# Kernel optimization log

Hardware: AMD Instinct MI355X
Metric: run time of the kernel (lower is better)

The kernel has to match this reference:

```python
import jax, jax.numpy as jnp
import numpy as np

B = 262144
N_FEAT = 256
N_D = 64
N_A = 64
N_OUT = N_D + N_A  # 128
N_STEPS = 3
N_STEP_DEP = 2
VBS = 1024
GAMMA = 1.3
EPS_BN = 1e-5
SQRT_HALF = float(np.sqrt(0.5))


def _xavier(key, shape):
    fan_in, fan_out = shape[-2], shape[-1]
    return (jax.random.normal(key, shape) * np.sqrt(2.0 / (fan_in + fan_out))).astype(jnp.float32)


def setup_inputs() -> dict:
    key = jax.random.key(0)
    ks = jax.random.split(key, 8)
    return {
        "x": jax.random.normal(ks[0], (B, N_FEAT), dtype=jnp.float32),
        "bn0_g": jnp.ones((N_FEAT,), jnp.float32),
        "bn0_b": jnp.zeros((N_FEAT,), jnp.float32),
        "W_sh0": _xavier(ks[1], (N_FEAT, 2 * N_OUT)),
        "g_sh0": jnp.ones((2 * N_OUT,), jnp.float32),
        "b_sh0": jnp.zeros((2 * N_OUT,), jnp.float32),
        "W_sh1": _xavier(ks[2], (N_OUT, 2 * N_OUT)),
        "g_sh1": jnp.ones((2 * N_OUT,), jnp.float32),
        "b_sh1": jnp.zeros((2 * N_OUT,), jnp.float32),
        "W_step": _xavier(ks[3], (N_STEPS, N_STEP_DEP, N_OUT, 2 * N_OUT)),
        "g_step": jnp.ones((N_STEPS, N_STEP_DEP, 2 * N_OUT), jnp.float32),
        "b_step": jnp.zeros((N_STEPS, N_STEP_DEP, 2 * N_OUT), jnp.float32),
        "W_att": _xavier(ks[4], (N_STEPS, N_A, N_FEAT)),
        "g_att": jnp.ones((N_STEPS, N_FEAT), jnp.float32),
        "b_att": jnp.zeros((N_STEPS, N_FEAT), jnp.float32),
    }


def batch_norm(x, g, b):
    # training-mode BN over the full batch (biased variance, as torch)
    mu = x.mean(0)
    var = ((x - mu) ** 2).mean(0)
    return (x - mu) * jax.lax.rsqrt(var + EPS_BN) * g + b


def ghost_bn(x, g, b):
    # split batch into virtual sub-batches of VBS and BN each chunk
    n, f = x.shape
    xr = x.reshape(n // VBS, VBS, f)
    mu = xr.mean(1, keepdims=True)
    var = ((xr - mu) ** 2).mean(1, keepdims=True)
    xn = (xr - mu) * jax.lax.rsqrt(var + EPS_BN)
    return xn.reshape(n, f) * g + b


def sparsemax(z):
    zs = jnp.flip(jnp.sort(z, axis=-1), axis=-1)      # descending
    cs = jnp.cumsum(zs, axis=-1)
    n = z.shape[-1]
    k = jnp.arange(1, n + 1, dtype=z.dtype)
    support = (k * zs > cs - 1.0).astype(z.dtype)
    kz = support.sum(-1, keepdims=True)
    idx = jnp.clip(kz - 1.0, 0.0).astype(jnp.int32)
    tau = (jnp.take_along_axis(cs, idx, axis=-1) - 1.0) / kz
    return jnp.maximum(z - tau, 0.0)


def glu(x, W, g, b):
    h = ghost_bn(x @ W, g, b)
    h1, h2 = jnp.split(h, 2, axis=-1)
    return h1 * jax.nn.sigmoid(h2)


def feat_transformer(x, W_sh0, g_sh0, b_sh0, W_sh1, g_sh1, b_sh1, Wst, gst, bst):
    h = glu(x, W_sh0, g_sh0, b_sh0)
    h = (h + glu(h, W_sh1, g_sh1, b_sh1)) * SQRT_HALF
    for j in range(N_STEP_DEP):
        h = (h + glu(h, Wst[j], gst[j], bst[j])) * SQRT_HALF
    return h


def reference(x, bn0_g, bn0_b, W_sh0, g_sh0, b_sh0, W_sh1, g_sh1, b_sh1,
              W_step, g_step, b_step, W_att, g_att, b_att):
    x_bn = batch_norm(x, bn0_g, bn0_b)
    prior = jnp.ones((B, N_FEAT), x.dtype)
    h_a = jnp.zeros((B, N_A), x.dtype)
    d_out = jnp.zeros((B, N_D), x.dtype)
    sl = jnp.asarray(0.0, x.dtype)
    masks = []
    for s in range(N_STEPS):
        a = ghost_bn(h_a @ W_att[s], g_att[s], b_att[s])
        M = sparsemax(prior * a)
        masks.append(M)
        prior = prior * (GAMMA - M)
        h = feat_transformer(M * x_bn, W_sh0, g_sh0, b_sh0, W_sh1, g_sh1, b_sh1,
                             W_step[s], g_step[s], b_step[s])
        d_out = d_out + jax.nn.relu(h[:, :N_D])
        h_a = h[:, N_D:]
        sl = sl + (-M * jnp.log(M + 1e-15)).mean()
    sl = sl / N_STEPS
    return d_out, sl, jnp.stack(masks)
```

## Files before the change

kernel.cpp:

```cpp
#include <hip/hip_runtime.h>
#include <math.h>

#define B_ROWS 262144
#define GAMMA_C 1.3f
#define EPS_C 1e-5f
#define SQH_C 0.70710678118654752440f
#define SL_SCALE (1.0f/201326592.0f)

typedef _Float16 f16;
typedef f16 f16x8 __attribute__((ext_vector_type(8)));
typedef f16 f16x4 __attribute__((ext_vector_type(4)));
typedef float f32x4 __attribute__((ext_vector_type(4)));

__device__ __forceinline__ int SWZ(int row, int kb, int RB, int MSK) {
  return row * RB + (kb ^ ((row & MSK) << 4));
}

__global__ void bn0_accum(const float* __restrict__ x, float* __restrict__ sums) {
  const int col = threadIdx.x;
  const size_t r0 = (size_t)blockIdx.x * 128;
  float s1 = 0.f, s2 = 0.f;
  for (int i = 0; i < 128; ++i) {
    float v = x[(r0 + i) * 256 + col];
    s1 += v; s2 += v * v;
  }
  atomicAdd(&sums[col * 2], s1);
  atomicAdd(&sums[col * 2 + 1], s2);
}

__global__ void bn0_final(const float* __restrict__ sums, const float* __restrict__ g,
                          const float* __restrict__ b, float* __restrict__ bnA,
                          float* __restrict__ bnB) {
  int c = threadIdx.x;
  float mu = sums[c * 2] * (1.f / B_ROWS);
  float var = sums[c * 2 + 1] * (1.f / B_ROWS) - mu * mu;
  float a = rsqrtf(var + EPS_C) * g[c];
  bnA[c] = a;
  bnB[c] = b[c] - mu * a;
}

__global__ void wprep(const float* __restrict__ src, f16* __restrict__ dst, int K) {
  int idx = blockIdx.x * 256 + threadIdx.x;
  int n = idx / K, k = idx - n * K;
  dst[idx] = (f16)src[(size_t)k * 256 + n];
}

__global__ void m0_kernel(const float* __restrict__ ba, float* __restrict__ m0v,
                          float* __restrict__ prior1v, float* __restrict__ slpart) {
  const int l = threadIdx.x;
  const int c0 = l << 2;
  float z[4];
#pragma unroll
  for (int j = 0; j < 4; ++j) z[j] = ba[c0 + j];
  float m = fmaxf(fmaxf(z[0], z[1]), fmaxf(z[2], z[3]));
#pragma unroll
  for (int d = 1; d < 64; d <<= 1) m = fmaxf(m, __shfl_xor(m, d));
  float lo = m - 1.f, hi = m;
  for (int it = 0; it < 24; ++it) {
    float tau = 0.5f * (lo + hi);
    float s = fmaxf(z[0] - tau, 0.f) + fmaxf(z[1] - tau, 0.f) +
              fmaxf(z[2] - tau, 0.f) + fmaxf(z[3] - tau, 0.f);
#pragma unroll
    for (int d = 1; d < 64; d <<= 1) s += __shfl_xor(s, d);
    if (s > 1.f) lo = tau; else hi = tau;
  }
  const float tau = 0.5f * (lo + hi);
  float ent = 0.f;
#pragma unroll
  for (int j = 0; j < 4; ++j) {
    float M = fmaxf(z[j] - tau, 0.f);
    m0v[c0 + j] = M;
    prior1v[c0 + j] = GAMMA_C - M;
    ent -= M * __logf(M + 1e-15f);
  }
#pragma unroll
  for (int d = 1; d < 64; d <<= 1) ent += __shfl_xor(ent, d);
  if (l == 0) slpart[512] = ent * (262144.f * SL_SCALE);
}

__global__ void mx0_kernel(const float* __restrict__ x, const float* __restrict__ m0v,
                           const float* __restrict__ bnA, const float* __restrict__ bnB,
                           float* __restrict__ mk, f16* __restrict__ Mx) {
  __shared__ float sm[256], sa[256], sb[256];
  const int tid = threadIdx.x;
  sm[tid] = m0v[tid]; sa[tid] = bnA[tid]; sb[tid] = bnB[tid];
  __syncthreads();
  const size_t r = (size_t)blockIdx.x * 8 + (tid >> 5);
  const int c0 = (tid & 31) << 3;
  const float* xp = x + r * 256 + c0;
  f32x4 x0 = *(const f32x4*)xp;
  f32x4 x1 = *(const f32x4*)(xp + 4);
  float* mp = mk + r * 256 + c0;
  f16x8 mxv;
#pragma unroll
  for (int j = 0; j < 4; ++j) {
    mp[j] = sm[c0 + j];
    mp[4 + j] = sm[c0 + 4 + j];
    mxv[j] = (f16)(sm[c0 + j] * (x0[j] * sa[c0 + j] + sb[c0 + j]));
    mxv[4 + j] = (f16)(sm[c0 + 4 + j] * (x1[j] * sa[c0 + 4 + j] + sb[c0 + 4 + j]));
  }
  *(f16x8*)(Mx + r * 256 + c0) = mxv;
}

template <int KD, int RESID, int DOUT>
__launch_bounds__(1024, 4)
__global__ void fglu(const f16* __restrict__ Ag, const f16* __restrict__ Wt,
                     const float* __restrict__ gv, const float* __restrict__ bv,
                     f16* __restrict__ ho, float* __restrict__ dout, int s) {
  constexpr int KS = KD / 32;
  constexpr int RB = KD * 2;
  constexpr int MSK = (RB / 16 - 1) < 31 ? (RB / 16 - 1) : 31;
  constexpr int SPT = (KD == 256) ? 2 : 1;
  constexpr int TPR = KD / 8;
  __shared__ __align__(16) f16 sA[64 * KD];
  __shared__ float sS1[512], sS2[512], sAf[256], sBf[256];
  char* sAc = (char*)sA;
  const int tid = threadIdx.x;
  const int w = tid >> 6, l = tid & 63, lg = l >> 4, lc = l & 15;
  const int mw = w >> 3, nw = w & 7;
  const int c1 = nw * 16 + lc, c2 = c1 + 128;
  const int r0 = blockIdx.x << 10;

  f16x8 bf0[KS], bf1[KS];
#pragma unroll
  for (int ks = 0; ks < KS; ++ks) {
    bf0[ks] = *(const f16x8*)(Wt + (size_t)c1 * KD + ks * 32 + lg * 8);
    bf1[ks] = *(const f16x8*)(Wt + (size_t)c2 * KD + ks * 32 + lg * 8);
  }

  f16x8 pv[SPT];
  auto LDA = [&](int ch) {
#pragma unroll
    for (int p = 0; p < SPT; ++p) {
      int flat = p * 1024 + tid;
      int row = flat / TPR, kc = flat % TPR;
      pv[p] = *(const f16x8*)(Ag + (size_t)(r0 + ch * 64 + row) * KD + kc * 8);
    }
  };
  auto STA = [&]() {
#pragma unroll
    for (int p = 0; p < SPT; ++p) {
      int flat = p * 1024 + tid;
      int row = flat / TPR, kc = flat % TPR;
      *(f16x8*)(sAc + SWZ(row, kc * 16, RB, MSK)) = pv[p];
    }
  };

  float st1a = 0.f, st2a = 0.f, st1b = 0.f, st2b = 0.f;
  LDA(0);
  for (int ch = 0; ch < 16; ++ch) {
    __syncthreads();
    STA();
    __syncthreads();
    if (ch < 15) LDA(ch + 1);
#pragma unroll
    for (int mt = 0; mt < 2; ++mt) {
      f32x4 a0 = {0.f,0.f,0.f,0.f}, a1 = {0.f,0.f,0.f,0.f};
      const int ar = mw * 32 + mt * 16 + lc;
#pragma unroll
      for (int ks = 0; ks < KS; ++ks) {
        f16x8 af = *(const f16x8*)(sAc + SWZ(ar, ks * 64 + lg * 16, RB, MSK));
        a0 = __builtin_amdgcn_mfma_f32_16x16x32_f16(af, bf0[ks], a0, 0, 0, 0);
        a1 = __builtin_amdgcn_mfma_f32_16x16x32_f16(af, bf1[ks], a1, 0, 0, 0);
      }
#pragma unroll
      for (int j = 0; j < 4; ++j) {
        st1a += a0[j]; st2a += a0[j] * a0[j];
        st1b += a1[j]; st2b += a1[j] * a1[j];
      }
    }
  }
  st1a += __shfl_xor(st1a, 16); st1a += __shfl_xor(st1a, 32);
  st2a += __shfl_xor(st2a, 16); st2a += __shfl_xor(st2a, 32);
  st1b += __shfl_xor(st1b, 16); st1b += __shfl_xor(st1b, 32);
  st2b += __shfl_xor(st2b, 16); st2b += __shfl_xor(st2b, 32);
  if (l < 16) {
    sS1[mw * 256 + c1] = st1a; sS2[mw * 256 + c1] = st2a;
    sS1[mw * 256 + c2] = st1b; sS2[mw * 256 + c2] = st2b;
  }
  __syncthreads();
  if (tid < 256) {
    float s1 = sS1[tid] + sS1[256 + tid];
    float s2 = sS2[tid] + sS2[256 + tid];
    float mu = s1 * (1.f / 1024.f);
    float var = s2 * (1.f / 1024.f) - mu * mu;
    float a = rsqrtf(var + EPS_C) * gv[tid];
    sAf[tid] = a; sBf[tid] = bv[tid] - mu * a;
  }
  __syncthreads();
  const float bA1 = sAf[c1], bO1 = sBf[c1], bA2 = sAf[c2], bO2 = sBf[c2];

  LDA(0);
  for (int ch = 0; ch < 16; ++ch) {
    __syncthreads();
    STA();
    __syncthreads();
    if (ch < 15) LDA(ch + 1);
#pragma unroll
    for (int mt = 0; mt < 2; ++mt) {
      f32x4 a0 = {0.f,0.f,0.f,0.f}, a1 = {0.f,0.f,0.f,0.f};
      const int ar = mw * 32 + mt * 16 + lc;
#pragma unroll
      for (int ks = 0; ks < KS; ++ks) {
        f16x8 af = *(const f16x8*)(sAc + SWZ(ar, ks * 64 + lg * 16, RB, MSK));
        a0 = __builtin_amdgcn_mfma_f32_16x16x32_f16(af, bf0[ks], a0, 0, 0, 0);
        a1 = __builtin_amdgcn_mfma_f32_16x16x32_f16(af, bf1[ks], a1, 0, 0, 0);
      }
#pragma unroll
      for (int j = 0; j < 4; ++j) {
        float g1 = a0[j] * bA1 + bO1;
        float g2 = a1[j] * bA2 + bO2;
        float hv = g1 / (1.f + __expf(-g2));
        const int rl = mw * 32 + mt * 16 + lg * 4 + j;
        if (RESID) {
          f16 hp = *(const f16*)(sAc + SWZ(rl, c1 * 2, RB, MSK));
          hv = (hv + (float)hp) * SQH_C;
        }
        if (DOUT && nw < 4) {
          float rv = fmaxf(hv, 0.f);
          float* dp = dout + (size_t)(r0 + ch * 64 + rl) * 64 + c1;
          if (s == 0) *dp = rv; else *dp += rv;
        }
        ho[(size_t)(r0 + ch * 64 + rl) * 128 + c1] = (f16)hv;
      }
    }
  }
}

template <int SMODE>
__launch_bounds__(512)
__global__ void attmask(const f16* __restrict__ h1, const f16* __restrict__ Wt,
                        const float* __restrict__ ga, const float* __restrict__ ba,
                        const float* __restrict__ bnA, const float* __restrict__ bnB,
                        const float* __restrict__ prior1v, const f16* __restrict__ prin,
                        f16* __restrict__ prout, const float* __restrict__ x,
                        float* __restrict__ mk, f16* __restrict__ Mx,
                        float* __restrict__ slpart) {
  __shared__ f16 sW[256 * 64];
  __shared__ f16 sA[128 * 64];
  __shared__ float sS1[256], sS2[256], sAf[256], sBf[256], sbA[256], sbB[256], spv[256];
  __shared__ float sEnt[8];
  char* sWc = (char*)sW;
  char* sAc = (char*)sA;
  const int tid = threadIdx.x;
  const int vb = blockIdx.x;
  const int r0 = vb << 10;
  const int w = tid >> 6, l = tid & 63, lc = l & 15, lg = l >> 4;
  if (tid < 256) {
    sS1[tid] = 0.f; sS2[tid] = 0.f;
    sbA[tid] = bnA[tid]; sbB[tid] = bnB[tid];
    if (SMODE == 1) spv[tid] = prior1v[tid];
  }
#pragma unroll
  for (int it = 0; it < 4; ++it) {
    int flat = it * 512 + tid;
    int rw = flat >> 3, kc = flat & 7;
    *(f16x8*)(sWc + SWZ(rw, kc * 16, 128, 7)) = *(const f16x8*)(Wt + rw * 64 + kc * 8);
  }
  const int arow = tid >> 3, akc = tid & 7;
  const f16* aB = h1 + (size_t)(r0 + arow) * 128 + 64 + akc * 8;
  float ent = 0.f;

  for (int pass = 0; pass < 2; ++pass) {
    float st1[16], st2[16];
#pragma unroll
    for (int t = 0; t < 16; ++t) { st1[t] = 0.f; st2[t] = 0.f; }
    f16x8 pv0 = *(const f16x8*)(aB);
    f16x8 pv1 = *(const f16x8*)(aB + (size_t)64 * 128);
    for (int ch = 0; ch < 8; ++ch) {
      __syncthreads();
      *(f16x8*)(sAc + SWZ(arow, akc * 16, 128, 7)) = pv0;
      *(f16x8*)(sAc + SWZ(arow + 64, akc * 16, 128, 7)) = pv1;
      __syncthreads();
      if (ch + 1 < 8) {
        pv0 = *(const f16x8*)(aB + (size_t)(ch + 1) * 128 * 128);
        pv1 = *(const f16x8*)(aB + (size_t)((ch + 1) * 128 + 64) * 128);
      }
      f16x8 af0 = *(const f16x8*)(sAc + SWZ(w * 16 + lc, lg * 16, 128, 7));
      f16x8 af1 = *(const f16x8*)(sAc + SWZ(w * 16 + lc, 64 + lg * 16, 128, 7));
      const int rb = r0 + ch * 128 + w * 16;
      f32x4 z[16];
#pragma unroll
      for (int t = 0; t < 16; ++t) {
        f16x8 b0 = *(const f16x8*)(sWc + SWZ(t * 16 + lc, lg * 16, 128, 7));
        f16x8 b1 = *(const f16x8*)(sWc + SWZ(t * 16 + lc, 64 + lg * 16, 128, 7));
        f32x4 acc = {0.f, 0.f, 0.f, 0.f};
        acc = __builtin_amdgcn_mfma_f32_16x16x32_f16(af0, b0, acc, 0, 0, 0);
        acc = __builtin_amdgcn_mfma_f32_16x16x32_f16(af1, b1, acc, 0, 0, 0);
        if (pass == 0) {
          float s1 = 0.f, s2 = 0.f;
#pragma unroll
          for (int j = 0; j < 4; ++j) { float v = acc[j]; s1 += v; s2 += v * v; }
          st1[t] += s1; st2[t] += s2;
        } else {
          const int c = t * 16 + lc;
          const float a = sAf[c], bb = sBf[c];
#pragma unroll
          for (int j = 0; j < 4; ++j) {
            float pr;
            if (SMODE == 1) pr = spv[c];
            else pr = (float)prin[(size_t)(rb + lg * 4 + j) * 256 + c];
            z[t][j] = (acc[j] * a + bb) * pr;
          }
        }
      }
      if (pass == 1) {
        f32x4 mj, lo, hi;
#pragma unroll
        for (int j = 0; j < 4; ++j) {
          float m = z[0][j];
#pragma unroll
          for (int t = 1; t < 16; ++t) m = fmaxf(m, z[t][j]);
          mj[j] = m;
        }
#pragma unroll
        for (int d = 1; d < 16; d <<= 1)
#pragma unroll
          for (int j = 0; j < 4; ++j) mj[j] = fmaxf(mj[j], __shfl_xor(mj[j], d));
#pragma unroll
        for (int j = 0; j < 4; ++j) { lo[j] = mj[j] - 1.f; hi[j] = mj[j]; }
        for (int itb = 0; itb < 20; ++itb) {
          f32x4 tau, sv;
#pragma unroll
          for (int j = 0; j < 4; ++j) { tau[j] = 0.5f * (lo[j] + hi[j]); sv[j] = 0.f; }
#pragma unroll
          for (int t = 0; t < 16; ++t)
#pragma unroll
            for (int j = 0; j < 4; ++j) sv[j] += fmaxf(z[t][j] - tau[j], 0.f);
#pragma unroll
          for (int d = 1; d < 16; d <<= 1)
#pragma unroll
            for (int j = 0; j < 4; ++j) sv[j] += __shfl_xor(sv[j], d);
#pragma unroll
          for (int j = 0; j < 4; ++j) { if (sv[j] > 1.f) lo[j] = tau[j]; else hi[j] = tau[j]; }
        }
        f32x4 tau;
#pragma unroll
        for (int j = 0; j < 4; ++j) tau[j] = 0.5f * (lo[j] + hi[j]);
#pragma unroll
        for (int t = 0; t < 16; ++t) {
          const int c = t * 16 + lc;
#pragma unroll
          for (int j = 0; j < 4; ++j) {
            const size_t r = (size_t)(rb + lg * 4 + j);
            float Mv = fmaxf(z[t][j] - tau[j], 0.f);
            mk[r * 256 + c] = Mv;
            ent -= Mv * __logf(Mv + 1e-15f);
            float xb = x[r * 256 + c] * sbA[c] + sbB[c];
            Mx[r * 256 + c] = (f16)(Mv * xb);
            if (SMODE == 1) prout[r * 256 + c] = (f16)(spv[c] * (GAMMA_C - Mv));
          }
        }
      }
    }
    if (pass == 0) {
#pragma unroll
      for (int t = 0; t < 16; ++t) {
        float v1 = st1[t], v2 = st2[t];
        v1 += __shfl_xor(v1, 16); v2 += __shfl_xor(v2, 16);
        v1 += __shfl_xor(v1, 32); v2 += __shfl_xor(v2, 32);
        if (l < 16) {
          atomicAdd(&sS1[t * 16 + lc], v1);
          atomicAdd(&sS2[t * 16 + lc], v2);
        }
      }
      __syncthreads();
      if (tid < 256) {
        float mu = sS1[tid] * (1.f / 1024.f);
        float var = sS2[tid] * (1.f / 1024.f) - mu * mu;
        float a = rsqrtf(var + EPS_C) * ga[tid];
        sAf[tid] = a;
        sBf[tid] = ba[tid] - mu * a;
      }
      __syncthreads();
    }
  }
#pragma unroll
  for (int d = 1; d < 64; d <<= 1) ent += __shfl_xor(ent, d);
  if (l == 0) sEnt[w] = ent;
  __syncthreads();
  if (tid == 0) {
    float t = 0.f;
#pragma unroll
    for (int i = 0; i < 8; ++i) t += sEnt[i];
    slpart[(SMODE - 1) * 256 + vb] = t * SL_SCALE;
  }
}

__global__ void sl_reduce(const float* __restrict__ part, float* __restrict__ out, int n) {
  __shared__ float sm[256];
  float s = 0.f;
  for (int i = threadIdx.x; i < n; i += 256) s += part[i];
  sm[threadIdx.x] = s;
  __syncthreads();
  for (int d = 128; d > 0; d >>= 1) {
    if ((int)threadIdx.x < d) sm[threadIdx.x] += sm[threadIdx.x + d];
    __syncthreads();
  }
  if (threadIdx.x == 0) out[0] = sm[0];
}

extern "C" void kernel_launch(void* const* d_in, const int* in_sizes, int n_in,
                              void* d_out, int out_size, void* d_ws, size_t ws_size,
                              hipStream_t stream) {
  (void)in_sizes; (void)n_in; (void)out_size; (void)ws_size;
  const float* x    = (const float*)d_in[0];
  const float* bn0g = (const float*)d_in[1];
  const float* bn0b = (const float*)d_in[2];
  const float* Wsh0 = (const float*)d_in[3];
  const float* gsh0 = (const float*)d_in[4];
  const float* bsh0 = (const float*)d_in[5];
  const float* Wsh1 = (const float*)d_in[6];
  const float* gsh1 = (const float*)d_in[7];
  const float* bsh1 = (const float*)d_in[8];
  const float* Wstep = (const float*)d_in[9];
  const float* gstep = (const float*)d_in[10];
  const float* bstep = (const float*)d_in[11];
  const float* Watt = (const float*)d_in[12];
  const float* gatt = (const float*)d_in[13];
  const float* batt = (const float*)d_in[14];

  float* dout = (float*)d_out;
  float* slo = dout + (size_t)B_ROWS * 64;
  float* masks = slo + 1;

  char* ws = (char*)d_ws;
  size_t off = 0;
  auto carve = [&](size_t bytes) -> char* {
    char* p = ws + off;
    off += (bytes + 255) & ~(size_t)255;
    return p;
  };
  f16* wt_att   = (f16*)carve((size_t)3 * 256 * 64 * 2);
  f16* wt_sh0   = (f16*)carve((size_t)256 * 256 * 2);
  f16* wt_sh1   = (f16*)carve((size_t)256 * 128 * 2);
  f16* wt_step  = (f16*)carve((size_t)6 * 256 * 128 * 2);
  float* bn0sum = (float*)carve(512 * 4);
  float* bnA    = (float*)carve(256 * 4);
  float* bnB    = (float*)carve(256 * 4);
  float* m0v    = (float*)carve(256 * 4);
  float* prior1v= (float*)carve(256 * 4);
  float* slpart = (float*)carve(513 * 4);
  f16* prior    = (f16*)carve((size_t)B_ROWS * 256 * 2);
  f16* Mx       = (f16*)carve((size_t)B_ROWS * 256 * 2);
  f16* h0       = (f16*)carve((size_t)B_ROWS * 128 * 2);
  f16* h1       = (f16*)carve((size_t)B_ROWS * 128 * 2);

  hipMemsetAsync(bn0sum, 0, 512 * 4, stream);
  bn0_accum<<<2048, 256, 0, stream>>>(x, bn0sum);
  bn0_final<<<1, 256, 0, stream>>>(bn0sum, bn0g, bn0b, bnA, bnB);
  for (int s = 1; s < 3; ++s)
    wprep<<<64, 256, 0, stream>>>(Watt + (size_t)s * 64 * 256, wt_att + (size_t)s * 256 * 64, 64);
  wprep<<<256, 256, 0, stream>>>(Wsh0, wt_sh0, 256);
  wprep<<<128, 256, 0, stream>>>(Wsh1, wt_sh1, 128);
  for (int i = 0; i < 6; ++i)
    wprep<<<128, 256, 0, stream>>>(Wstep + (size_t)i * 128 * 256, wt_step + (size_t)i * 256 * 128, 128);
  m0_kernel<<<1, 64, 0, stream>>>(batt, m0v, prior1v, slpart);
  mx0_kernel<<<B_ROWS / 8, 256, 0, stream>>>(x, m0v, bnA, bnB, masks, Mx);

  for (int s = 0; s < 3; ++s) {
    if (s == 1)
      attmask<1><<<256, 512, 0, stream>>>(h1, wt_att + (size_t)1 * 256 * 64,
                                          gatt + 256, batt + 256, bnA, bnB,
                                          prior1v, nullptr, prior, x,
                                          masks + (size_t)1 * B_ROWS * 256, Mx, slpart);
    else if (s == 2)
      attmask<2><<<256, 512, 0, stream>>>(h1, wt_att + (size_t)2 * 256 * 64,
                                          gatt + 512, batt + 512, bnA, bnB,
                                          nullptr, prior, nullptr, x,
                                          masks + (size_t)2 * B_ROWS * 256, Mx, slpart);
    fglu<256, 0, 0><<<256, 1024, 0, stream>>>(Mx, wt_sh0, gsh0, bsh0, h0, nullptr, s);
    fglu<128, 1, 0><<<256, 1024, 0, stream>>>(h0, wt_sh1, gsh1, bsh1, h1, nullptr, s);
    fglu<128, 1, 0><<<256, 1024, 0, stream>>>(h1, wt_step + (size_t)(s * 2 + 0) * 256 * 128,
                                              gstep + (s * 2 + 0) * 256, bstep + (s * 2 + 0) * 256,
                                              h0, nullptr, s);
    fglu<128, 1, 1><<<256, 1024, 0, stream>>>(h0, wt_step + (size_t)(s * 2 + 1) * 256 * 128,
                                              gstep + (s * 2 + 1) * 256, bstep + (s * 2 + 1) * 256,
                                              h1, dout, s);
  }
  sl_reduce<<<1, 256, 0, stream>>>(slpart, slo, 513);
}
```

Measured before the change: 1.908 ms.

## Split fused GLU blocks by output column half and merge weight-prep launches

Each fglu block previously computed all 128 output columns for 1024 rows using 1024 threads. Now two 512-thread blocks share a row chunk, each computing half the GLU columns, which doubles the grid to 512 blocks so all CUs get work and occupancy improves. In exchange, every A tile is loaded and staged twice, raising global and LDS traffic. The many small wprep launches are also merged into a single launch to cut launch overhead.

```diff
diff --git a/kernel.cpp b/kernel.cpp
--- a/kernel.cpp
+++ b/kernel.cpp
@@ -39,8 +39,17 @@
   bnB[c] = b[c] - mu * a;
 }
 
-__global__ void wprep(const float* __restrict__ src, f16* __restrict__ dst, int K) {
-  int idx = blockIdx.x * 256 + threadIdx.x;
+__global__ void wprep_all(const float* __restrict__ Wsh0, const float* __restrict__ Wsh1,
+                          const float* __restrict__ Wstep, const float* __restrict__ Watt,
+                          f16* __restrict__ wt_sh0, f16* __restrict__ wt_sh1,
+                          f16* __restrict__ wt_step, f16* __restrict__ wt_att) {
+  int b = blockIdx.x;
+  const float* src; f16* dst; int K, lb;
+  if (b < 256)       { src = Wsh0; dst = wt_sh0; K = 256; lb = b; }
+  else if (b < 384)  { src = Wsh1; dst = wt_sh1; K = 128; lb = b - 256; }
+  else if (b < 1152) { int i = (b - 384) >> 7; src = Wstep + i * 32768; dst = wt_step + i * 32768; K = 128; lb = (b - 384) & 127; }
+  else               { int i = (b - 1152) >> 6; src = Watt + (size_t)(i + 1) * 16384; dst = wt_att + (size_t)(i + 1) * 16384; K = 64; lb = (b - 1152) & 63; }
+  int idx = lb * 256 + threadIdx.x;
   int n = idx / K, k = idx - n * K;
   dst[idx] = (f16)src[(size_t)k * 256 + n];
 }
@@ -103,23 +112,26 @@
 }
 
 template <int KD, int RESID, int DOUT>
-__launch_bounds__(1024, 4)
+__launch_bounds__(512, 4)
 __global__ void fglu(const f16* __restrict__ Ag, const f16* __restrict__ Wt,
                      const float* __restrict__ gv, const float* __restrict__ bv,
                      f16* __restrict__ ho, float* __restrict__ dout, int s) {
   constexpr int KS = KD / 32;
   constexpr int RB = KD * 2;
   constexpr int MSK = (RB / 16 - 1) < 31 ? (RB / 16 - 1) : 31;
-  constexpr int SPT = (KD == 256) ? 2 : 1;
   constexpr int TPR = KD / 8;
+  constexpr int SPT = 64 * TPR / 512;
   __shared__ __align__(16) f16 sA[64 * KD];
-  __shared__ float sS1[512], sS2[512], sAf[256], sBf[256];
+  __shared__ float sS1[256], sS2[256], sAf[128], sBf[128];
   char* sAc = (char*)sA;
   const int tid = threadIdx.x;
   const int w = tid >> 6, l = tid & 63, lg = l >> 4, lc = l & 15;
-  const int mw = w >> 3, nw = w & 7;
-  const int c1 = nw * 16 + lc, c2 = c1 + 128;
-  const int r0 = blockIdx.x << 10;
+  const int mw = w >> 2, nw = w & 3;
+  const int half = blockIdx.x & 1;
+  const int r0 = (blockIdx.x >> 1) << 10;
+  const int lc1 = nw * 16 + lc;
+  const int c1 = half * 64 + lc1;
+  const int c2 = c1 + 128;
 
   f16x8 bf0[KS], bf1[KS];
 #pragma unroll
@@ -132,7 +144,7 @@
   auto LDA = [&](int ch) {
 #pragma unroll
     for (int p = 0; p < SPT; ++p) {
-      int flat = p * 1024 + tid;
+      int flat = p * 512 + tid;
       int row = flat / TPR, kc = flat % TPR;
       pv[p] = *(const f16x8*)(Ag + (size_t)(r0 + ch * 64 + row) * KD + kc * 8);
     }
@@ -140,7 +152,7 @@
   auto STA = [&]() {
 #pragma unroll
     for (int p = 0; p < SPT; ++p) {
-      int flat = p * 1024 + tid;
+      int flat = p * 512 + tid;
       int row = flat / TPR, kc = flat % TPR;
       *(f16x8*)(sAc + SWZ(row, kc * 16, RB, MSK)) = pv[p];
     }
@@ -175,20 +187,22 @@
   st1b += __shfl_xor(st1b, 16); st1b += __shfl_xor(st1b, 32);
   st2b += __shfl_xor(st2b, 16); st2b += __shfl_xor(st2b, 32);
   if (l < 16) {
-    sS1[mw * 256 + c1] = st1a; sS2[mw * 256 + c1] = st2a;
-    sS1[mw * 256 + c2] = st1b; sS2[mw * 256 + c2] = st2b;
+    sS1[mw * 128 + lc1] = st1a;      sS2[mw * 128 + lc1] = st2a;
+    sS1[mw * 128 + 64 + lc1] = st1b; sS2[mw * 128 + 64 + lc1] = st2b;
   }
   __syncthreads();
-  if (tid < 256) {
-    float s1 = sS1[tid] + sS1[256 + tid];
-    float s2 = sS2[tid] + sS2[256 + tid];
+  if (tid < 128) {
+    float s1 = sS1[tid] + sS1[128 + tid];
+    float s2 = sS2[tid] + sS2[128 + tid];
+    int gcol = half * 64 + (tid < 64 ? tid : tid + 64);
     float mu = s1 * (1.f / 1024.f);
     float var = s2 * (1.f / 1024.f) - mu * mu;
-    float a = rsqrtf(var + EPS_C) * gv[tid];
-    sAf[tid] = a; sBf[tid] = bv[tid] - mu * a;
+    float a = rsqrtf(var + EPS_C) * gv[gcol];
+    sAf[tid] = a; sBf[tid] = bv[gcol] - mu * a;
   }
   __syncthreads();
-  const float bA1 = sAf[c1], bO1 = sBf[c1], bA2 = sAf[c2], bO2 = sBf[c2];
+  const float bA1 = sAf[lc1], bO1 = sBf[lc1];
+  const float bA2 = sAf[64 + lc1], bO2 = sBf[64 + lc1];
 
   LDA(0);
   for (int ch = 0; ch < 16; ++ch) {
@@ -216,7 +230,7 @@
           f16 hp = *(const f16*)(sAc + SWZ(rl, c1 * 2, RB, MSK));
           hv = (hv + (float)hp) * SQH_C;
         }
-        if (DOUT && nw < 4) {
+        if (DOUT && half == 0) {
           float rv = fmaxf(hv, 0.f);
           float* dp = dout + (size_t)(r0 + ch * 64 + rl) * 64 + c1;
           if (s == 0) *dp = rv; else *dp += rv;
@@ -449,12 +463,7 @@
   hipMemsetAsync(bn0sum, 0, 512 * 4, stream);
   bn0_accum<<<2048, 256, 0, stream>>>(x, bn0sum);
   bn0_final<<<1, 256, 0, stream>>>(bn0sum, bn0g, bn0b, bnA, bnB);
-  for (int s = 1; s < 3; ++s)
-    wprep<<<64, 256, 0, stream>>>(Watt + (size_t)s * 64 * 256, wt_att + (size_t)s * 256 * 64, 64);
-  wprep<<<256, 256, 0, stream>>>(Wsh0, wt_sh0, 256);
-  wprep<<<128, 256, 0, stream>>>(Wsh1, wt_sh1, 128);
-  for (int i = 0; i < 6; ++i)
-    wprep<<<128, 256, 0, stream>>>(Wstep + (size_t)i * 128 * 256, wt_step + (size_t)i * 256 * 128, 128);
+  wprep_all<<<1280, 256, 0, stream>>>(Wsh0, Wsh1, Wstep, Watt, wt_sh0, wt_sh1, wt_step, wt_att);
   m0_kernel<<<1, 64, 0, stream>>>(batt, m0v, prior1v, slpart);
   mx0_kernel<<<B_ROWS / 8, 256, 0, stream>>>(x, m0v, bnA, bnB, masks, Mx);
 
@@ -469,14 +478,14 @@
                                           gatt + 512, batt + 512, bnA, bnB,
                                           nullptr, prior, nullptr, x,
                                           masks + (size_t)2 * B_ROWS * 256, Mx, slpart);
-    fglu<256, 0, 0><<<256, 1024, 0, stream>>>(Mx, wt_sh0, gsh0, bsh0, h0, nullptr, s);
-    fglu<128, 1, 0><<<256, 1024, 0, stream>>>(h0, wt_sh1, gsh1, bsh1, h1, nullptr, s);
-    fglu<128, 1, 0><<<256, 1024, 0, stream>>>(h1, wt_step + (size_t)(s * 2 + 0) * 256 * 128,
-                                              gstep + (s * 2 + 0) * 256, bstep + (s * 2 + 0) * 256,
-                                              h0, nullptr, s);
-    fglu<128, 1, 1><<<256, 1024, 0, stream>>>(h0, wt_step + (size_t)(s * 2 + 1) * 256 * 128,
-                                              gstep + (s * 2 + 1) * 256, bstep + (s * 2 + 1) * 256,
-                                              h1, dout, s);
+    fglu<256, 0, 0><<<512, 512, 0, stream>>>(Mx, wt_sh0, gsh0, bsh0, h0, nullptr, s);
+    fglu<128, 1, 0><<<512, 512, 0, stream>>>(h0, wt_sh1, gsh1, bsh1, h1, nullptr, s);
+    fglu<128, 1, 0><<<512, 512, 0, stream>>>(h1, wt_step + (size_t)(s * 2 + 0) * 256 * 128,
+                                             gstep + (s * 2 + 0) * 256, bstep + (s * 2 + 0) * 256,
+                                             h0, nullptr, s);
+    fglu<128, 1, 1><<<512, 512, 0, stream>>>(h0, wt_step + (size_t)(s * 2 + 1) * 256 * 128,
+                                             gstep + (s * 2 + 1) * 256, bstep + (s * 2 + 1) * 256,
+                                             h1, dout, s);
   }
   sl_reduce<<<1, 256, 0, stream>>>(slpart, slo, 513);
 }
```

Result: slower. 1.962 ms (+2.9%).
